# Performance work log

Measured on AMD Instinct MI355X. Metric: run time of the kernel, lower is better.

The kernel has to match this reference:

```python
import jax, jax.numpy as jnp
import numpy as np

B, LQ, LK, D = 32, 2048, 2048, 256
TEMPERATURE = 16.0  # sqrt(D)
MASK_P = 0.15


def setup_inputs() -> dict:
    key = jax.random.key(0)
    kq, kk, kv, ks, km = jax.random.split(key, 5)
    q = jax.random.normal(kq, (B, LQ, D), dtype=jnp.float32)
    k = jax.random.normal(kk, (B, LK, D), dtype=jnp.float32)
    v = jax.random.normal(kv, (B, LK, D), dtype=jnp.float32)
    # random boolean masks (True = masked); low density so no row is fully masked
    src_mask = jax.random.bernoulli(ks, MASK_P, (B, LQ, LK))
    mel_mask = jax.random.bernoulli(km, MASK_P, (B, LQ, LK))
    return {"q": q, "k": k, "v": v, "src_mask": src_mask, "mel_mask": mel_mask}


def reference(q, k, v, src_mask, mel_mask):
    # attn = (q @ k^T) / temperature, shape [B, LQ, LK]
    attn = jnp.einsum("bqd,bkd->bqk", q, k) / TEMPERATURE
    # dual-mask path: mel_mask -> -inf before softmax, src_mask -> 0 after softmax
    attn = jnp.where(mel_mask, -jnp.inf, attn)
    attn = jax.nn.softmax(attn, axis=2)
    attn = jnp.where(src_mask, 0.0, attn)
    output = jnp.einsum("bqk,bkd->bqd", attn, v)
    return (output, attn)
```

## Files before the change

### kernel.cpp

```cpp
#include <hip/hip_runtime.h>
#include <hip/hip_bf16.h>
#include <cstdint>

#define B_   32
#define LQ_  2048
#define LK_  2048
#define D_   256
#define INV_T 0.0625f

typedef __attribute__((ext_vector_type(8))) short bf16x8;
typedef __attribute__((ext_vector_type(4))) float f32x4;

__device__ __forceinline__ unsigned short f2bf(float f) {
    union { float f; unsigned u; } a; a.f = f;
    unsigned u = a.u;
    unsigned r = (u + 0x7FFFu + ((u >> 16) & 1u)) >> 16;
    return (unsigned short)r;
}

__device__ __forceinline__ unsigned long long pack4bf(float a, float b, float c, float d) {
    return (unsigned long long)f2bf(a)
         | ((unsigned long long)f2bf(b) << 16)
         | ((unsigned long long)f2bf(c) << 32)
         | ((unsigned long long)f2bf(d) << 48);
}

__global__ __launch_bounds__(256) void qk_exp_kernel(
    const float* __restrict__ q, const float* __restrict__ kmat,
    const int* __restrict__ mel, float* __restrict__ attn,
    float* __restrict__ rowsum)
{
    const int id  = blockIdx.x;
    const int xcd = id & 7;
    const int idx = id >> 3;
    const int b   = xcd + 8 * (idx >> 8);
    const int t   = idx & 255;
    const int m0  = (t >> 4) * 128;
    const int n0  = (t & 15) * 128;

    __shared__ unsigned short As[128][72];
    __shared__ unsigned short Bs[128][72];

    const int tid  = threadIdx.x;
    const int wave = tid >> 6, lane = tid & 63;
    const int wm   = wave >> 1, wn = wave & 1;
    const int quad = lane >> 4, l16 = lane & 15;

    f32x4 acc[4][4];
#pragma unroll
    for (int i = 0; i < 4; ++i)
#pragma unroll
        for (int j = 0; j < 4; ++j) acc[i][j] = (f32x4)(0.0f);

    const float* qb = q    + (size_t)b * LQ_ * D_;
    const float* kb = kmat + (size_t)b * LK_ * D_;

    const int sr = tid >> 4;
    const int sc = (tid & 15) * 4;

    for (int kt = 0; kt < 4; ++kt) {
        const int kbase = kt * 64;
#pragma unroll
        for (int p = 0; p < 8; ++p) {
            const int row = sr + p * 16;
            float4 va = *(const float4*)&qb[(size_t)(m0 + row) * D_ + kbase + sc];
            float4 vb = *(const float4*)&kb[(size_t)(n0 + row) * D_ + kbase + sc];
            As[row][sc+0] = f2bf(va.x); As[row][sc+1] = f2bf(va.y);
            As[row][sc+2] = f2bf(va.z); As[row][sc+3] = f2bf(va.w);
            Bs[row][sc+0] = f2bf(vb.x); Bs[row][sc+1] = f2bf(vb.y);
            Bs[row][sc+2] = f2bf(vb.z); Bs[row][sc+3] = f2bf(vb.w);
        }
        __syncthreads();
#pragma unroll
        for (int ks = 0; ks < 2; ++ks) {
            bf16x8 af[4], bfr[4];
#pragma unroll
            for (int i = 0; i < 4; ++i)
                af[i] = *(const bf16x8*)&As[wm*64 + i*16 + l16][ks*32 + quad*8];
#pragma unroll
            for (int j = 0; j < 4; ++j)
                bfr[j] = *(const bf16x8*)&Bs[wn*64 + j*16 + l16][ks*32 + quad*8];
#pragma unroll
            for (int i = 0; i < 4; ++i)
#pragma unroll
                for (int j = 0; j < 4; ++j)
                    acc[i][j] = __builtin_amdgcn_mfma_f32_16x16x32_bf16(
                        af[i], bfr[j], acc[i][j], 0, 0, 0);
        }
        __syncthreads();
    }

    float*      attnB = attn + (size_t)b * LQ_ * LK_;
    const int*  melB  = mel  + (size_t)b * LQ_ * LK_;

    float rs[4][4];
#pragma unroll
    for (int i = 0; i < 4; ++i)
#pragma unroll
        for (int r = 0; r < 4; ++r) rs[i][r] = 0.0f;

#pragma unroll
    for (int i = 0; i < 4; ++i) {
#pragma unroll
        for (int j = 0; j < 4; ++j) {
#pragma unroll
            for (int r = 0; r < 4; ++r) {
                const int row = wm*64 + i*16 + quad*4 + r;
                const int col = wn*64 + j*16 + l16;
                const size_t gi = (size_t)(m0 + row) * LK_ + (n0 + col);
                float s = acc[i][j][r] * INV_T;
                float p = melB[gi] ? 0.0f : __expf(s);
                attnB[gi] = p;
                rs[i][r] += p;
            }
        }
    }

#pragma unroll
    for (int i = 0; i < 4; ++i) {
#pragma unroll
        for (int r = 0; r < 4; ++r) {
            float s = rs[i][r];
            s += __shfl_xor(s, 1);
            s += __shfl_xor(s, 2);
            s += __shfl_xor(s, 4);
            s += __shfl_xor(s, 8);
            if (l16 == 0) {
                const int row = wm*64 + i*16 + quad*4 + r;
                atomicAdd(&rowsum[(size_t)b * LQ_ + m0 + row], s);
            }
        }
    }
}


__device__ __forceinline__ const bf16x8* lds_frag(
    const unsigned short (*arr)[64], int row, int chunk) {
    const int key = (row ^ (row >> 3)) & 7;
    return (const bf16x8*)&arr[row][(chunk ^ key) << 3];
}

__device__ __forceinline__ int swz8(int row, int e) {
    return (e & 7) | ((((e >> 3) ^ row ^ (row >> 3)) & 7) << 3);
}

__global__ __launch_bounds__(256) void pv_norm_kernel(
    const float* __restrict__ v, const int* __restrict__ src,
    const float* __restrict__ rowsum, float* __restrict__ attn,
    float* __restrict__ out)
{
    const int id  = blockIdx.x;
    const int xcd = id & 7;
    const int idx = id >> 3;
    const int b   = xcd + 8 * (idx >> 5);
    const int m0  = (idx & 31) * 64;

    __shared__ unsigned short As[64][64];
    __shared__ unsigned short Vt[256][64];

    const int tid  = threadIdx.x;
    const int wave = tid >> 6, lane = tid & 63;
    const int wn   = wave;
    const int quad = lane >> 4, l16 = lane & 15;

    f32x4 acc[4][4];
#pragma unroll
    for (int i = 0; i < 4; ++i)
#pragma unroll
        for (int j = 0; j < 4; ++j) acc[i][j] = (f32x4)(0.0f);

    const float* vb    = v    + (size_t)b * LK_ * D_;
    float*       attnB = attn + (size_t)b * LQ_ * LK_;
    const int*   srcB  = src  + (size_t)b * LQ_ * LK_;

    const int sr = tid >> 4;
    const int sc = (tid & 15) * 4;

    float il[4];
#pragma unroll
    for (int p = 0; p < 4; ++p)
        il[p] = 1.0f / rowsum[(size_t)b * LQ_ + m0 + sr + p * 16];

    float4 pv_r[4]; int4 sv_r[4];
#pragma unroll
    for (int p = 0; p < 4; ++p) {
        const int row = sr + p * 16;
        const size_t gi = (size_t)(m0 + row) * LK_ + sc;
        pv_r[p] = *(const float4*)&attnB[gi];
        sv_r[p] = *(const int4*)&srcB[gi];
    }

    for (int kt = 0; kt < 32; ++kt) {
        const int k0 = kt * 64;

#pragma unroll
        for (int p = 0; p < 4; ++p) {
            const int row = sr + p * 16;
            const size_t gi = (size_t)(m0 + row) * LK_ + k0 + sc;
            const float ilp = il[p];
            float a0 = sv_r[p].x ? 0.0f : pv_r[p].x * ilp;
            float a1 = sv_r[p].y ? 0.0f : pv_r[p].y * ilp;
            float a2 = sv_r[p].z ? 0.0f : pv_r[p].z * ilp;
            float a3 = sv_r[p].w ? 0.0f : pv_r[p].w * ilp;
            float4 st; st.x = a0; st.y = a1; st.z = a2; st.w = a3;
            *(float4*)&attnB[gi] = st;
            *(unsigned long long*)&As[row][swz8(row, sc)] = pack4bf(a0, a1, a2, a3);
        }

#pragma unroll
        for (int p = 0; p < 4; ++p) {
            const int bi  = tid + p * 256;
            const int bkv = (bi >> 6) * 4;
            const int bn  = (bi & 63) * 4;
            const float* s0 = &vb[(size_t)(k0 + bkv) * D_ + bn];
            float4 r0 = *(const float4*)(s0);
            float4 r1 = *(const float4*)(s0 + D_);
            float4 r2 = *(const float4*)(s0 + 2 * D_);
            float4 r3 = *(const float4*)(s0 + 3 * D_);
            *(unsigned long long*)&Vt[bn+0][swz8(bn+0, bkv)] = pack4bf(r0.x, r1.x, r2.x, r3.x);
            *(unsigned long long*)&Vt[bn+1][swz8(bn+1, bkv)] = pack4bf(r0.y, r1.y, r2.y, r3.y);
            *(unsigned long long*)&Vt[bn+2][swz8(bn+2, bkv)] = pack4bf(r0.z, r1.z, r2.z, r3.z);
            *(unsigned long long*)&Vt[bn+3][swz8(bn+3, bkv)] = pack4bf(r0.w, r1.w, r2.w, r3.w);
        }

        if (kt < 31) {
#pragma unroll
            for (int p = 0; p < 4; ++p) {
                const int row = sr + p * 16;
                const size_t gi = (size_t)(m0 + row) * LK_ + (k0 + 64) + sc;
                pv_r[p] = *(const float4*)&attnB[gi];
                sv_r[p] = *(const int4*)&srcB[gi];
            }
        }
        __syncthreads();

#pragma unroll
        for (int ks = 0; ks < 2; ++ks) {
            bf16x8 af[4], bfr[4];
            const int chunk = ks * 4 + quad;
#pragma unroll
            for (int i = 0; i < 4; ++i)
                af[i] = *lds_frag(As, i*16 + l16, chunk);
#pragma unroll
            for (int j = 0; j < 4; ++j)
                bfr[j] = *lds_frag(Vt, wn*64 + j*16 + l16, chunk);
#pragma unroll
            for (int i = 0; i < 4; ++i)
#pragma unroll
                for (int j = 0; j < 4; ++j)
                    acc[i][j] = __builtin_amdgcn_mfma_f32_16x16x32_bf16(
                        af[i], bfr[j], acc[i][j], 0, 0, 0);
        }
        __syncthreads();
    }

    float* outB = out + (size_t)b * LQ_ * D_;
#pragma unroll
    for (int i = 0; i < 4; ++i) {
#pragma unroll
        for (int j = 0; j < 4; ++j) {
#pragma unroll
            for (int r = 0; r < 4; ++r) {
                const int row = i*16 + quad*4 + r;
                const int col = wn*64 + j*16 + l16;
                outB[(size_t)(m0 + row) * D_ + col] = acc[i][j][r];
            }
        }
    }
}

extern "C" void kernel_launch(void* const* d_in, const int* in_sizes, int n_in,
                              void* d_out, int out_size, void* d_ws, size_t ws_size,
                              hipStream_t stream) {
    const float* q        = (const float*)d_in[0];
    const float* k        = (const float*)d_in[1];
    const float* v        = (const float*)d_in[2];
    const int*   src_mask = (const int*)d_in[3];
    const int*   mel_mask = (const int*)d_in[4];

    float* out  = (float*)d_out;
    float* attn = out + (size_t)B_ * LQ_ * D_;
    float* rowsum = (float*)d_ws;

    hipMemsetAsync(rowsum, 0, (size_t)B_ * LQ_ * sizeof(float), stream);

    qk_exp_kernel<<<dim3(16 * 16 * B_), 256, 0, stream>>>(
        q, k, mel_mask, attn, rowsum);

    pv_norm_kernel<<<dim3((LQ_ / 64) * B_), 256, 0, stream>>>(
        v, src_mask, rowsum, attn, out);
}
```

Measured before the change: 1.734 ms.

## Stage QK epilogue through LDS for vectorized mask loads and attn stores

The QK^T kernel's epilogue now writes scaled scores into a swizzled LDS buffer that shares storage with the operand tiles, in two 64-row halves. Threads then read back row-contiguous chunks, do float4 loads of the mel mask and float4 stores of exp(attn), and issue one atomicAdd per row group. The aim is to replace scattered scalar global accesses from the MFMA fragment layout with coalesced vector accesses and fewer atomics. Operand staging also packs four bf16 values into one 64-bit LDS store, using the library bf16 conversion. The cost is extra LDS traffic and additional barriers in the epilogue.

```diff
diff --git a/kernel.cpp b/kernel.cpp
--- a/kernel.cpp
+++ b/kernel.cpp
@@ -12,18 +12,27 @@
 typedef __attribute__((ext_vector_type(4))) float f32x4;
 
 __device__ __forceinline__ unsigned short f2bf(float f) {
-    union { float f; unsigned u; } a; a.f = f;
-    unsigned u = a.u;
-    unsigned r = (u + 0x7FFFu + ((u >> 16) & 1u)) >> 16;
-    return (unsigned short)r;
+    __hip_bfloat16 h = __float2bfloat16(f);
+    unsigned short u;
+    __builtin_memcpy(&u, &h, 2);
+    return u;
 }
 
 __device__ __forceinline__ unsigned long long pack4bf(float a, float b, float c, float d) {
-    return (unsigned long long)f2bf(a)
-         | ((unsigned long long)f2bf(b) << 16)
-         | ((unsigned long long)f2bf(c) << 32)
-         | ((unsigned long long)f2bf(d) << 48);
-}
+    unsigned int lo = (unsigned int)f2bf(a) | ((unsigned int)f2bf(b) << 16);
+    unsigned int hi = (unsigned int)f2bf(c) | ((unsigned int)f2bf(d) << 16);
+    return (unsigned long long)lo | ((unsigned long long)hi << 32);
+}
+
+struct QkSmem {
+    union {
+        struct {
+            unsigned short A[128][72];
+            unsigned short Bv[128][72];
+        } st;
+        float ep[64][128];
+    };
+};
 
 __global__ __launch_bounds__(256) void qk_exp_kernel(
     const float* __restrict__ q, const float* __restrict__ kmat,
@@ -38,8 +47,7 @@
     const int m0  = (t >> 4) * 128;
     const int n0  = (t & 15) * 128;
 
-    __shared__ unsigned short As[128][72];
-    __shared__ unsigned short Bs[128][72];
+    __shared__ QkSmem sm;
 
     const int tid  = threadIdx.x;
     const int wave = tid >> 6, lane = tid & 63;
@@ -65,10 +73,8 @@
             const int row = sr + p * 16;
             float4 va = *(const float4*)&qb[(size_t)(m0 + row) * D_ + kbase + sc];
             float4 vb = *(const float4*)&kb[(size_t)(n0 + row) * D_ + kbase + sc];
-            As[row][sc+0] = f2bf(va.x); As[row][sc+1] = f2bf(va.y);
-            As[row][sc+2] = f2bf(va.z); As[row][sc+3] = f2bf(va.w);
-            Bs[row][sc+0] = f2bf(vb.x); Bs[row][sc+1] = f2bf(vb.y);
-            Bs[row][sc+2] = f2bf(vb.z); Bs[row][sc+3] = f2bf(vb.w);
+            *(unsigned long long*)&sm.st.A[row][sc]  = pack4bf(va.x, va.y, va.z, va.w);
+            *(unsigned long long*)&sm.st.Bv[row][sc] = pack4bf(vb.x, vb.y, vb.z, vb.w);
         }
         __syncthreads();
 #pragma unroll
@@ -76,10 +82,10 @@
             bf16x8 af[4], bfr[4];
 #pragma unroll
             for (int i = 0; i < 4; ++i)
-                af[i] = *(const bf16x8*)&As[wm*64 + i*16 + l16][ks*32 + quad*8];
+                af[i] = *(const bf16x8*)&sm.st.A[wm*64 + i*16 + l16][ks*32 + quad*8];
 #pragma unroll
             for (int j = 0; j < 4; ++j)
-                bfr[j] = *(const bf16x8*)&Bs[wn*64 + j*16 + l16][ks*32 + quad*8];
+                bfr[j] = *(const bf16x8*)&sm.st.Bv[wn*64 + j*16 + l16][ks*32 + quad*8];
 #pragma unroll
             for (int i = 0; i < 4; ++i)
 #pragma unroll
@@ -93,43 +99,50 @@
     float*      attnB = attn + (size_t)b * LQ_ * LK_;
     const int*  melB  = mel  + (size_t)b * LQ_ * LK_;
 
-    float rs[4][4];
-#pragma unroll
-    for (int i = 0; i < 4; ++i)
-#pragma unroll
-        for (int r = 0; r < 4; ++r) rs[i][r] = 0.0f;
-
-#pragma unroll
-    for (int i = 0; i < 4; ++i) {
-#pragma unroll
-        for (int j = 0; j < 4; ++j) {
-#pragma unroll
-            for (int r = 0; r < 4; ++r) {
-                const int row = wm*64 + i*16 + quad*4 + r;
-                const int col = wn*64 + j*16 + l16;
-                const size_t gi = (size_t)(m0 + row) * LK_ + (n0 + col);
-                float s = acc[i][j][r] * INV_T;
-                float p = melB[gi] ? 0.0f : __expf(s);
-                attnB[gi] = p;
-                rs[i][r] += p;
+    for (int c = 0; c < 2; ++c) {
+        if (wm == c) {
+#pragma unroll
+            for (int i = 0; i < 4; ++i) {
+#pragma unroll
+                for (int j = 0; j < 4; ++j) {
+#pragma unroll
+                    for (int r = 0; r < 4; ++r) {
+                        const int row = i*16 + quad*4 + r;
+                        const int col = wn*64 + j*16 + l16;
+                        const int ch  = (col >> 2) ^ (row & 7);
+                        sm.ep[row][(ch << 2) | (col & 3)] = acc[i][j][r] * INV_T;
+                    }
+                }
             }
         }
-    }
-
-#pragma unroll
-    for (int i = 0; i < 4; ++i) {
-#pragma unroll
-        for (int r = 0; r < 4; ++r) {
-            float s = rs[i][r];
-            s += __shfl_xor(s, 1);
-            s += __shfl_xor(s, 2);
-            s += __shfl_xor(s, 4);
-            s += __shfl_xor(s, 8);
-            if (l16 == 0) {
-                const int row = wm*64 + i*16 + quad*4 + r;
-                atomicAdd(&rowsum[(size_t)b * LQ_ + m0 + row], s);
+        __syncthreads();
+
+        {
+            const int row  = tid >> 2;
+            const int g    = tid & 3;
+            const int grow = m0 + c*64 + row;
+            const size_t gbase = (size_t)grow * LK_ + n0;
+            float rsum = 0.0f;
+#pragma unroll
+            for (int c4 = 0; c4 < 8; ++c4) {
+                const int col = g*32 + c4*4;
+                const int ch  = (col >> 2) ^ (row & 7);
+                f32x4 s4 = *(const f32x4*)&sm.ep[row][ch << 2];
+                int4  mv = *(const int4*)&melB[gbase + col];
+                float p0 = mv.x ? 0.0f : __expf(s4.x);
+                float p1 = mv.y ? 0.0f : __expf(s4.y);
+                float p2 = mv.z ? 0.0f : __expf(s4.z);
+                float p3 = mv.w ? 0.0f : __expf(s4.w);
+                float4 st; st.x = p0; st.y = p1; st.z = p2; st.w = p3;
+                *(float4*)&attnB[gbase + col] = st;
+                rsum += (p0 + p1) + (p2 + p3);
             }
-        }
+            rsum += __shfl_xor(rsum, 1);
+            rsum += __shfl_xor(rsum, 2);
+            if (g == 0)
+                atomicAdd(&rowsum[(size_t)b * LQ_ + grow], rsum);
+        }
+        __syncthreads();
     }
 }
 
```

Result: slower. 1.787 ms (+3.1%).
